# Performance work log

Measured on AMD Instinct MI355X. Metric: run time of the kernel, lower is better.

The kernel has to match this reference:

```python
import jax, jax.numpy as jnp
import numpy as np
from jax import lax

B, N, M = 2, 16384, 4096
C1, C2 = 128, 256
H1, H2 = 256, 128  # mlp = [C1+C2, 256, 128]


def setup_inputs() -> dict:
    key = jax.random.key(0)
    ks = jax.random.split(key, 8)
    return {
        "unknown": jax.random.normal(ks[0], (B, N, 3), jnp.float32),
        "known": jax.random.normal(ks[1], (B, M, 3), jnp.float32),
        "unknow_feats": jax.random.normal(ks[2], (B, C1, N), jnp.float32),
        "known_feats": jax.random.normal(ks[3], (B, C2, M), jnp.float32),
        "W1": jax.random.normal(ks[4], (H1, C1 + C2), jnp.float32) * 0.05,
        "b1": jnp.zeros((H1,), jnp.float32),
        "W2": jax.random.normal(ks[5], (H2, H1), jnp.float32) * 0.05,
        "b2": jnp.zeros((H2,), jnp.float32),
    }


def reference(unknown, known, unknow_feats, known_feats, W1, b1, W2, b2):
    # Pairwise squared distances (B, n, m) via ||a||^2 + ||b||^2 - 2 a.b
    d2 = (
        jnp.sum(unknown * unknown, -1)[:, :, None]
        + jnp.sum(known * known, -1)[:, None, :]
        - 2.0 * jnp.einsum("bnd,bmd->bnm", unknown, known)
    )
    # 3 nearest neighbors
    neg_d2, idx = lax.top_k(-d2, 3)  # (B, n, 3)
    dist = jnp.sqrt(jnp.maximum(-neg_d2, 0.0))  # pointops returns sqrt distances
    dist_recip = 1.0 / (dist + 1e-8)
    weight = dist_recip / jnp.sum(dist_recip, axis=2, keepdims=True)  # (B, n, 3)
    # Gather neighbor features (B, C2, n, 3) and inverse-distance weighted sum
    gathered = jax.vmap(lambda f, i: f[:, i])(known_feats, idx)
    interpolated = jnp.sum(gathered * weight[:, None, :, :], axis=-1)  # (B, C2, n)
    new_features = jnp.concatenate([interpolated, unknow_feats], axis=1)  # (B, C1+C2, n)
    # Shared MLP (1x1 convs, bn=False -> conv bias + ReLU)
    h = jax.nn.relu(jnp.einsum("oc,bcn->bon", W1, new_features) + b1[None, :, None])
    out = jax.nn.relu(jnp.einsum("oc,bcn->bon", W2, h) + b2[None, :, None])
    return out  # (B, mlp[-1], n)
```

## Files before the change

### kernel.cpp

```cpp
#include <hip/hip_runtime.h>
#include <hip/hip_bf16.h>

#define BB 2
#define NN 16384
#define MM 4096
#define C1 128
#define C2 256
#define CIN 384
#define H1 256
#define H2 128
#define XROW 392
#define HROW 264

typedef __attribute__((ext_vector_type(8))) short bf16x8;
typedef __attribute__((ext_vector_type(4))) float f32x4;
typedef __attribute__((ext_vector_type(2))) float f32x2;
typedef __attribute__((ext_vector_type(8))) float f32x8;

__device__ __forceinline__ short f32_to_bf16(float x) {
    unsigned u = __float_as_uint(x);
    u += 0x7fffu + ((u >> 16) & 1u);
    return (short)(u >> 16);
}
__device__ __forceinline__ float bf16_to_f32(unsigned short u) {
    union { unsigned u; float f; } c; c.u = ((unsigned)u) << 16; return c.f;
}
__device__ __forceinline__ unsigned pack_bf16x2(float a, float b) {
    __hip_bfloat162 h = __float22bfloat162_rn(make_float2(a, b));
    union { __hip_bfloat162 h; unsigned u; } cv;
    cv.h = h;
    return cv.u;
}
__device__ __forceinline__ f32x2 score2(f32x2 ax2, f32x2 ay2, f32x2 az2,
                                        f32x2 kx, f32x2 ky, f32x2 kz, f32x2 kn) {
    f32x2 t = ay2 * ky;
    t = __builtin_elementwise_fma(ax2, kx, t);
    t = __builtin_elementwise_fma(az2, kz, t);
    return t + kn;
}

__global__ __launch_bounds__(256) void prep_kernel(
    const float* __restrict__ KF, unsigned short* __restrict__ KT16,
    const float* __restrict__ W1, const float* __restrict__ W2,
    short* __restrict__ W1b, short* __restrict__ W2b,
    const float* __restrict__ known, float* __restrict__ kpk8)
{
    const int bx  = blockIdx.x;
    const int tid = threadIdx.x;
    if (bx < 2048) {
        __shared__ float tl[32][33];
        const int b  = bx >> 10;
        const int c0 = ((bx >> 7) & 7) * 32;
        const int m0 = (bx & 127) * 32;
        const int tx = tid & 31;
        const int ty = tid >> 5;
        #pragma unroll
        for (int r = 0; r < 4; ++r) {
            int c = ty + r * 8;
            tl[c][tx] = KF[((size_t)b * C2 + c0 + c) * MM + m0 + tx];
        }
        __syncthreads();
        #pragma unroll
        for (int r = 0; r < 4; ++r) {
            int m = ty + r * 8;
            KT16[((size_t)b * MM + m0 + m) * C2 + c0 + tx] =
                (unsigned short)f32_to_bf16(tl[tx][m]);
        }
    } else if (bx < 2432) {
        int i = (bx - 2048) * 256 + tid;
        if (i < H1 * CIN) W1b[i] = f32_to_bf16(W1[i]);
        if (i < H2 * H1)  W2b[i] = f32_to_bf16(W2[i]);
    } else {
        int i = (bx - 2432) * 256 + tid;
        if (i < BB * MM) {
            float x = known[3 * i + 0], y = known[3 * i + 1], z = known[3 * i + 2];
            float n = fmaf(x, x, fmaf(y, y, z * z));
            int g = i >> 1, j = i & 1;
            float* base = kpk8 + (size_t)g * 8;
            base[0 + j] = x; base[2 + j] = y; base[4 + j] = z; base[6 + j] = n;
        }
    }
}

__global__ __launch_bounds__(1024, 8) void fused_knn_mlp_kernel(
    const float* __restrict__ unknown,
    const float* __restrict__ kpk8,
    const float* __restrict__ unknow_feats,
    const unsigned short* __restrict__ KT16,
    const short* __restrict__ W1b, const float* __restrict__ b1,
    const short* __restrict__ W2b, const float* __restrict__ b2,
    float* __restrict__ out)
{
    __shared__ float pdv[16][64][3];
    __shared__ float vf[64];
    __shared__ float msc[64][8];
    __shared__ int   mid[64][8];
    __shared__ int   cnt[64];
    __shared__ int   IsL[64 * 3];
    __shared__ float WsL[64 * 3];
    __shared__ short XH[32][XROW];
    __shared__ short Hs[32][HROW];

    const int bx    = blockIdx.x;
    const int tid   = threadIdx.x;
    const int lane  = tid & 63;
    const int w     = __builtin_amdgcn_readfirstlane(tid >> 6);
    const int b     = bx >> 8;
    const int qbase = (bx & 255) * 64;
    const int n     = qbase + lane;

    if (tid < 64) cnt[tid] = 0;

    {
        const float ux = unknown[((size_t)b * NN + n) * 3 + 0];
        const float uy = unknown[((size_t)b * NN + n) * 3 + 1];
        const float uz = unknown[((size_t)b * NN + n) * 3 + 2];
        const f32x2 ax2 = {-2.f * ux, -2.f * ux};
        const f32x2 ay2 = {-2.f * uy, -2.f * uy};
        const f32x2 az2 = {-2.f * uz, -2.f * uz};
        const float un = fmaf(ux, ux, fmaf(uy, uy, uz * uz));

        const int gbase = w * 128;
        const float* __restrict__ kp = kpk8 + ((size_t)b * (MM / 2) + gbase) * 8;

        float va0 = 3e38f, va1 = 3e38f, va2 = 3e38f;
        float vb0 = 3e38f, vb1 = 3e38f, vb2 = 3e38f;
        #pragma unroll 4
        for (int g = 0; g < 128; ++g) {
            const f32x8 G = *(const f32x8*)(kp + (size_t)g * 8);
            const f32x2 kx = __builtin_shufflevector(G, G, 0, 1);
            const f32x2 ky = __builtin_shufflevector(G, G, 2, 3);
            const f32x2 kz = __builtin_shufflevector(G, G, 4, 5);
            const f32x2 kn = __builtin_shufflevector(G, G, 6, 7);
            const f32x2 sc2 = score2(ax2, ay2, az2, kx, ky, kz, kn);
            float sa = sc2.x;
            va2 = __builtin_amdgcn_fmed3f(va1, sa, va2);
            va1 = __builtin_amdgcn_fmed3f(va0, sa, va1);
            va0 = fminf(sa, va0);
            float sb = sc2.y;
            vb2 = __builtin_amdgcn_fmed3f(vb1, sb, vb2);
            vb1 = __builtin_amdgcn_fmed3f(vb0, sb, vb1);
            vb0 = fminf(sb, vb0);
        }
        {
            float bv[3] = {vb0, vb1, vb2};
            #pragma unroll
            for (int k = 0; k < 3; ++k) {
                float d = bv[k];
                va2 = __builtin_amdgcn_fmed3f(va1, d, va2);
                va1 = __builtin_amdgcn_fmed3f(va0, d, va1);
                va0 = fminf(d, va0);
            }
        }
        pdv[w][lane][0] = va0; pdv[w][lane][1] = va1; pdv[w][lane][2] = va2;
        __syncthreads();

        if (tid < 64) {
            float r0 = 3e38f, r1 = 3e38f, r2 = 3e38f;
            #pragma unroll
            for (int ww = 0; ww < 16; ++ww) {
                #pragma unroll
                for (int k = 0; k < 3; ++k) {
                    float d = pdv[ww][tid][k];
                    r2 = __builtin_amdgcn_fmed3f(r1, d, r2);
                    r1 = __builtin_amdgcn_fmed3f(r0, d, r1);
                    r0 = fminf(d, r0);
                }
            }
            vf[tid] = r2;
        }
        __syncthreads();

        const float v2f = vf[lane];
        #pragma unroll 4
        for (int g = 0; g < 128; ++g) {
            const f32x8 G = *(const f32x8*)(kp + (size_t)g * 8);
            const f32x2 kx = __builtin_shufflevector(G, G, 0, 1);
            const f32x2 ky = __builtin_shufflevector(G, G, 2, 3);
            const f32x2 kz = __builtin_shufflevector(G, G, 4, 5);
            const f32x2 kn = __builtin_shufflevector(G, G, 6, 7);
            const f32x2 sc2 = score2(ax2, ay2, az2, kx, ky, kz, kn);
            if (fminf(sc2.x, sc2.y) <= v2f) {
                if (sc2.x <= v2f) {
                    int c = atomicAdd(&cnt[lane], 1);
                    if (c < 8) { msc[lane][c] = sc2.x; mid[lane][c] = (gbase + g) * 2; }
                }
                if (sc2.y <= v2f) {
                    int c = atomicAdd(&cnt[lane], 1);
                    if (c < 8) { msc[lane][c] = sc2.y; mid[lane][c] = (gbase + g) * 2 + 1; }
                }
            }
        }
        __syncthreads();

        if (tid < 64) {
            const int c = cnt[tid] < 8 ? cnt[tid] : 8;
            float r0 = 3e38f, r1 = 3e38f, r2 = 3e38f;
            int   q0 = 0x7FFFFFFF, q1 = 0x7FFFFFFF, q2 = 0x7FFFFFFF;
            #pragma unroll
            for (int k = 0; k < 8; ++k) {
                float d = (k < c) ? msc[tid][k] : 3e38f;
                int   j = (k < c) ? mid[tid][k] : 0x7FFFFFFF;
                const bool lt0 = (d < r0) || (d == r0 && j < q0);
                const bool lt1 = (d < r1) || (d == r1 && j < q1);
                const bool lt2 = (d < r2) || (d == r2 && j < q2);
                float nr2 = lt1 ? r1 : (lt2 ? d : r2);
                int   nq2 = lt1 ? q1 : (lt2 ? j : q2);
                float nr1 = lt0 ? r0 : (lt1 ? d : r1);
                int   nq1 = lt0 ? q0 : (lt1 ? j : q1);
                float nr0 = lt0 ? d : r0;
                int   nq0 = lt0 ? j : q0;
                r0 = nr0; r1 = nr1; r2 = nr2; q0 = nq0; q1 = nq1; q2 = nq2;
            }
            float d0 = sqrtf(fmaxf(r0 + un, 0.f));
            float d1 = sqrtf(fmaxf(r1 + un, 0.f));
            float d2 = sqrtf(fmaxf(r2 + un, 0.f));
            float i0 = 1.f / (d0 + 1e-8f);
            float i1 = 1.f / (d1 + 1e-8f);
            float i2 = 1.f / (d2 + 1e-8f);
            float s  = i0 + i1 + i2;
            IsL[tid * 3 + 0] = q0; IsL[tid * 3 + 1] = q1; IsL[tid * 3 + 2] = q2;
            WsL[tid * 3 + 0] = i0 / s; WsL[tid * 3 + 1] = i1 / s; WsL[tid * 3 + 2] = i2 / s;
        }
    }
    __syncthreads();

    const unsigned short* KTb = KT16 + (size_t)b * MM * C2;
    const int lr = lane & 15;
    const int lq = lane >> 4;
    const int c4 = lane << 2;

    for (int tile = 0; tile < 2; ++tile) {
        const int pbase = tile * 32;

        {
            ushort4 g[2][3];
            #pragma unroll
            for (int j = 0; j < 2; ++j) {
                const int pi = (pbase + 2 * w + j) * 3;
                g[j][0] = *(const ushort4*)(KTb + (size_t)IsL[pi + 0] * C2 + c4);
                g[j][1] = *(const ushort4*)(KTb + (size_t)IsL[pi + 1] * C2 + c4);
                g[j][2] = *(const ushort4*)(KTb + (size_t)IsL[pi + 2] * C2 + c4);
            }
            #pragma unroll
            for (int j = 0; j < 2; ++j) {
                const int pl = 2 * w + j;
                const int pi = (pbase + pl) * 3;
                const float w0 = WsL[pi + 0], w1 = WsL[pi + 1], w2 = WsL[pi + 2];
                float vx = fmaf(w0, bf16_to_f32(g[j][0].x), fmaf(w1, bf16_to_f32(g[j][1].x), w2 * bf16_to_f32(g[j][2].x)));
                float vy = fmaf(w0, bf16_to_f32(g[j][0].y), fmaf(w1, bf16_to_f32(g[j][1].y), w2 * bf16_to_f32(g[j][2].y)));
                float vz = fmaf(w0, bf16_to_f32(g[j][0].z), fmaf(w1, bf16_to_f32(g[j][1].z), w2 * bf16_to_f32(g[j][2].z)));
                float vw = fmaf(w0, bf16_to_f32(g[j][0].w), fmaf(w1, bf16_to_f32(g[j][1].w), w2 * bf16_to_f32(g[j][2].w)));
                uint2 pk;
                pk.x = pack_bf16x2(vx, vy);
                pk.y = pack_bf16x2(vz, vw);
                *(uint2*)&XH[pl][c4] = pk;
            }
            const float* UFb = unknow_feats + (size_t)b * C1 * NN + qbase + pbase;
            const int cc = tid >> 3;
            const int nq = (tid & 7) << 2;
            const float4 f = *(const float4*)(UFb + (size_t)cc * NN + nq);
            XH[nq + 0][C2 + cc] = f32_to_bf16(f.x);
            XH[nq + 1][C2 + cc] = f32_to_bf16(f.y);
            XH[nq + 2][C2 + cc] = f32_to_bf16(f.z);
            XH[nq + 3][C2 + cc] = f32_to_bf16(f.w);
        }
        __syncthreads();

        f32x4 acc1[2];
        acc1[0] = (f32x4){0.f, 0.f, 0.f, 0.f};
        acc1[1] = (f32x4){0.f, 0.f, 0.f, 0.f};
        #pragma unroll 4
        for (int k0 = 0; k0 < CIN; k0 += 32) {
            bf16x8 a  = *(const bf16x8*)(W1b + (size_t)(w * 16 + lr) * CIN + k0 + lq * 8);
            bf16x8 x0 = *(bf16x8*)&XH[lr][k0 + lq * 8];
            bf16x8 x1 = *(bf16x8*)&XH[16 + lr][k0 + lq * 8];
            acc1[0] = __builtin_amdgcn_mfma_f32_16x16x32_bf16(a, x0, acc1[0], 0, 0, 0);
            acc1[1] = __builtin_amdgcn_mfma_f32_16x16x32_bf16(a, x1, acc1[1], 0, 0, 0);
        }
        {
            const int ob = w * 16 + lq * 4;
            float bb0 = b1[ob + 0], bb1 = b1[ob + 1], bb2 = b1[ob + 2], bb3 = b1[ob + 3];
            #pragma unroll
            for (int p = 0; p < 2; ++p) {
                uint2 pk;
                pk.x = pack_bf16x2(fmaxf(acc1[p].x + bb0, 0.f),
                                   fmaxf(acc1[p].y + bb1, 0.f));
                pk.y = pack_bf16x2(fmaxf(acc1[p].z + bb2, 0.f),
                                   fmaxf(acc1[p].w + bb3, 0.f));
                *(uint2*)&Hs[p * 16 + lr][ob] = pk;
            }
        }
        __syncthreads();

        {
            const int r0 = (w & 7) * 16;
            const int pg = (w >> 3) * 16;
            f32x4 acc2 = (f32x4){0.f, 0.f, 0.f, 0.f};
            #pragma unroll 4
            for (int k0 = 0; k0 < H1; k0 += 32) {
                bf16x8 a2 = *(const bf16x8*)(W2b + (size_t)(r0 + lr) * H1 + k0 + lq * 8);
                bf16x8 h  = *(bf16x8*)&Hs[pg + lr][k0 + lq * 8];
                acc2 = __builtin_amdgcn_mfma_f32_16x16x32_bf16(a2, h, acc2, 0, 0, 0);
            }
            const int nn = qbase + pbase + pg + lr;
            #pragma unroll
            for (int r = 0; r < 4; ++r) {
                const int o = r0 + lq * 4 + r;
                out[((size_t)b * H2 + o) * NN + nn] =
                    fmaxf(((const float*)&acc2)[r] + b2[o], 0.f);
            }
        }
        __syncthreads();
    }
}

extern "C" void kernel_launch(void* const* d_in, const int* in_sizes, int n_in,
                              void* d_out, int out_size, void* d_ws, size_t ws_size,
                              hipStream_t stream) {
    const float* unknown      = (const float*)d_in[0];
    const float* known        = (const float*)d_in[1];
    const float* unknow_feats = (const float*)d_in[2];
    const float* known_feats  = (const float*)d_in[3];
    const float* W1           = (const float*)d_in[4];
    const float* b1           = (const float*)d_in[5];
    const float* W2           = (const float*)d_in[6];
    const float* b2           = (const float*)d_in[7];
    float* out = (float*)d_out;

    char* ws = (char*)d_ws;
    short*          W1b  = (short*)(ws);
    short*          W2b  = (short*)(ws + 196608);
    float*          kpk8 = (float*)(ws + 262144);
    unsigned short* KT16 = (unsigned short*)(ws + 393216);

    prep_kernel<<<2464, 256, 0, stream>>>(
        known_feats, KT16, W1, W2, W1b, W2b, known, kpk8);

    fused_knn_mlp_kernel<<<512, 1024, 0, stream>>>(
        unknown, kpk8, unknow_feats, KT16, W1b, b1, W2b, b2, out);
}
```

Before: 162.5 us.

## Halve block to 512 threads, alias LDS buffers, prefetch unknown features early

The fused kNN+MLP kernel moves from 1024 to 512 threads per block. Each wave now scans 256 known-point pairs instead of 128, gathers 4 points instead of 2, and computes 32 output rows per MFMA tile in the first layer. The kNN scratch, the XH input tile and the hidden activations now share one LDS union, and Hs is dropped by writing H into XH after an extra barrier. Unknown features for both tiles are prefetched into registers at kernel start so their load latency overlaps the kNN search. This lowers LDS footprint and may allow more blocks per CU, at the cost of more registers per thread and longer serial work per wave.

After: 176.7 us. 8.7% more time.

```diff
diff --git a/kernel.cpp b/kernel.cpp
--- a/kernel.cpp
+++ b/kernel.cpp
@@ -10,7 +10,6 @@
 #define H1 256
 #define H2 128
 #define XROW 392
-#define HROW 264
 
 typedef __attribute__((ext_vector_type(8))) short bf16x8;
 typedef __attribute__((ext_vector_type(4))) float f32x4;
@@ -82,7 +81,7 @@
     }
 }
 
-__global__ __launch_bounds__(1024, 8) void fused_knn_mlp_kernel(
+__global__ __launch_bounds__(512, 8) void fused_knn_mlp_kernel(
     const float* __restrict__ unknown,
     const float* __restrict__ kpk8,
     const float* __restrict__ unknow_feats,
@@ -91,15 +90,19 @@
     const short* __restrict__ W2b, const float* __restrict__ b2,
     float* __restrict__ out)
 {
-    __shared__ float pdv[16][64][3];
-    __shared__ float vf[64];
-    __shared__ float msc[64][8];
-    __shared__ int   mid[64][8];
-    __shared__ int   cnt[64];
+    union SharedU {
+        struct {
+            float pdv[8][64][3];
+            float vf[64];
+            float msc[64][8];
+            int   mid[64][8];
+            int   cnt[64];
+        } p1;
+        short XH[32][XROW];
+    };
+    __shared__ SharedU S;
     __shared__ int   IsL[64 * 3];
     __shared__ float WsL[64 * 3];
-    __shared__ short XH[32][XROW];
-    __shared__ short Hs[32][HROW];
 
     const int bx    = blockIdx.x;
     const int tid   = threadIdx.x;
@@ -109,7 +112,19 @@
     const int qbase = (bx & 255) * 64;
     const int n     = qbase + lane;
 
-    if (tid < 64) cnt[tid] = 0;
+    float4 uf[4];
+    {
+        const float* UFb = unknow_feats + (size_t)b * C1 * NN + qbase;
+        #pragma unroll
+        for (int i = 0; i < 4; ++i) {
+            int e  = (i & 1) * 512 + tid;
+            int cc = e >> 3;
+            int nq = ((e & 7) << 2) + (i >> 1) * 32;
+            uf[i] = *(const float4*)(UFb + (size_t)cc * NN + nq);
+        }
+    }
+
+    if (tid < 64) S.p1.cnt[tid] = 0;
 
     {
         const float ux = unknown[((size_t)b * NN + n) * 3 + 0];
@@ -120,13 +135,13 @@
         const f32x2 az2 = {-2.f * uz, -2.f * uz};
         const float un = fmaf(ux, ux, fmaf(uy, uy, uz * uz));
 
-        const int gbase = w * 128;
+        const int gbase = w * 256;
         const float* __restrict__ kp = kpk8 + ((size_t)b * (MM / 2) + gbase) * 8;
 
         float va0 = 3e38f, va1 = 3e38f, va2 = 3e38f;
         float vb0 = 3e38f, vb1 = 3e38f, vb2 = 3e38f;
         #pragma unroll 4
-        for (int g = 0; g < 128; ++g) {
+        for (int g = 0; g < 256; ++g) {
             const f32x8 G = *(const f32x8*)(kp + (size_t)g * 8);
             const f32x2 kx = __builtin_shufflevector(G, G, 0, 1);
             const f32x2 ky = __builtin_shufflevector(G, G, 2, 3);
@@ -152,28 +167,28 @@
                 va0 = fminf(d, va0);
             }
         }
-        pdv[w][lane][0] = va0; pdv[w][lane][1] = va1; pdv[w][lane][2] = va2;
+        S.p1.pdv[w][lane][0] = va0; S.p1.pdv[w][lane][1] = va1; S.p1.pdv[w][lane][2] = va2;
         __syncthreads();
 
         if (tid < 64) {
             float r0 = 3e38f, r1 = 3e38f, r2 = 3e38f;
             #pragma unroll
-            for (int ww = 0; ww < 16; ++ww) {
+            for (int ww = 0; ww < 8; ++ww) {
                 #pragma unroll
                 for (int k = 0; k < 3; ++k) {
-                    float d = pdv[ww][tid][k];
+                    float d = S.p1.pdv[ww][tid][k];
                     r2 = __builtin_amdgcn_fmed3f(r1, d, r2);
                     r1 = __builtin_amdgcn_fmed3f(r0, d, r1);
                     r0 = fminf(d, r0);
                 }
             }
-            vf[tid] = r2;
-        }
-        __syncthreads();
-
-        const float v2f = vf[lane];
+            S.p1.vf[tid] = r2;
+        }
+        __syncthreads();
+
+        const float v2f = S.p1.vf[lane];
         #pragma unroll 4
-        for (int g = 0; g < 128; ++g) {
+        for (int g = 0; g < 256; ++g) {
             const f32x8 G = *(const f32x8*)(kp + (size_t)g * 8);
             const f32x2 kx = __builtin_shufflevector(G, G, 0, 1);
             const f32x2 ky = __builtin_shufflevector(G, G, 2, 3);
@@ -182,25 +197,25 @@
             const f32x2 sc2 = score2(ax2, ay2, az2, kx, ky, kz, kn);
             if (fminf(sc2.x, sc2.y) <= v2f) {
                 if (sc2.x <= v2f) {
-                    int c = atomicAdd(&cnt[lane], 1);
-                    if (c < 8) { msc[lane][c] = sc2.x; mid[lane][c] = (gbase + g) * 2; }
+                    int c = atomicAdd(&S.p1.cnt[lane], 1);
+                    if (c < 8) { S.p1.msc[lane][c] = sc2.x; S.p1.mid[lane][c] = (gbase + g) * 2; }
                 }
                 if (sc2.y <= v2f) {
-                    int c = atomicAdd(&cnt[lane], 1);
-                    if (c < 8) { msc[lane][c] = sc2.y; mid[lane][c] = (gbase + g) * 2 + 1; }
+                    int c = atomicAdd(&S.p1.cnt[lane], 1);
+                    if (c < 8) { S.p1.msc[lane][c] = sc2.y; S.p1.mid[lane][c] = (gbase + g) * 2 + 1; }
                 }
             }
         }
         __syncthreads();
 
         if (tid < 64) {
-            const int c = cnt[tid] < 8 ? cnt[tid] : 8;
+            const int c = S.p1.cnt[tid] < 8 ? S.p1.cnt[tid] : 8;
             float r0 = 3e38f, r1 = 3e38f, r2 = 3e38f;
             int   q0 = 0x7FFFFFFF, q1 = 0x7FFFFFFF, q2 = 0x7FFFFFFF;
             #pragma unroll
             for (int k = 0; k < 8; ++k) {
-                float d = (k < c) ? msc[tid][k] : 3e38f;
-                int   j = (k < c) ? mid[tid][k] : 0x7FFFFFFF;
+                float d = (k < c) ? S.p1.msc[tid][k] : 3e38f;
+                int   j = (k < c) ? S.p1.mid[tid][k] : 0x7FFFFFFF;
                 const bool lt0 = (d < r0) || (d == r0 && j < q0);
                 const bool lt1 = (d < r1) || (d == r1 && j < q1);
                 const bool lt2 = (d < r2) || (d == r2 && j < q2);
@@ -234,17 +249,28 @@
         const int pbase = tile * 32;
 
         {
-            ushort4 g[2][3];
-            #pragma unroll
-            for (int j = 0; j < 2; ++j) {
-                const int pi = (pbase + 2 * w + j) * 3;
+            ushort4 g[4][3];
+            #pragma unroll
+            for (int j = 0; j < 4; ++j) {
+                const int pi = (pbase + 4 * w + j) * 3;
                 g[j][0] = *(const ushort4*)(KTb + (size_t)IsL[pi + 0] * C2 + c4);
                 g[j][1] = *(const ushort4*)(KTb + (size_t)IsL[pi + 1] * C2 + c4);
                 g[j][2] = *(const ushort4*)(KTb + (size_t)IsL[pi + 2] * C2 + c4);
             }
             #pragma unroll
-            for (int j = 0; j < 2; ++j) {
-                const int pl = 2 * w + j;
+            for (int i = 0; i < 2; ++i) {
+                const float4 f = uf[tile * 2 + i];
+                int e  = i * 512 + tid;
+                int cc = e >> 3;
+                int nq = (e & 7) << 2;
+                S.XH[nq + 0][C2 + cc] = f32_to_bf16(f.x);
+                S.XH[nq + 1][C2 + cc] = f32_to_bf16(f.y);
+                S.XH[nq + 2][C2 + cc] = f32_to_bf16(f.z);
+                S.XH[nq + 3][C2 + cc] = f32_to_bf16(f.w);
+            }
+            #pragma unroll
+            for (int j = 0; j < 4; ++j) {
+                const int pl = 4 * w + j;
                 const int pi = (pbase + pl) * 3;
                 const float w0 = WsL[pi + 0], w1 = WsL[pi + 1], w2 = WsL[pi + 2];
                 float vx = fmaf(w0, bf16_to_f32(g[j][0].x), fmaf(w1, bf16_to_f32(g[j][1].x), w2 * bf16_to_f32(g[j][2].x)));
@@ -254,61 +280,70 @@
                 uint2 pk;
                 pk.x = pack_bf16x2(vx, vy);
                 pk.y = pack_bf16x2(vz, vw);
-                *(uint2*)&XH[pl][c4] = pk;
-            }
-            const float* UFb = unknow_feats + (size_t)b * C1 * NN + qbase + pbase;
-            const int cc = tid >> 3;
-            const int nq = (tid & 7) << 2;
-            const float4 f = *(const float4*)(UFb + (size_t)cc * NN + nq);
-            XH[nq + 0][C2 + cc] = f32_to_bf16(f.x);
-            XH[nq + 1][C2 + cc] = f32_to_bf16(f.y);
-            XH[nq + 2][C2 + cc] = f32_to_bf16(f.z);
-            XH[nq + 3][C2 + cc] = f32_to_bf16(f.w);
-        }
-        __syncthreads();
-
-        f32x4 acc1[2];
-        acc1[0] = (f32x4){0.f, 0.f, 0.f, 0.f};
-        acc1[1] = (f32x4){0.f, 0.f, 0.f, 0.f};
+                *(uint2*)&S.XH[pl][c4] = pk;
+            }
+        }
+        __syncthreads();
+
+        f32x4 acc1[2][2];
+        #pragma unroll
+        for (int t = 0; t < 2; ++t)
+            #pragma unroll
+            for (int p = 0; p < 2; ++p) acc1[t][p] = (f32x4){0.f, 0.f, 0.f, 0.f};
         #pragma unroll 4
         for (int k0 = 0; k0 < CIN; k0 += 32) {
-            bf16x8 a  = *(const bf16x8*)(W1b + (size_t)(w * 16 + lr) * CIN + k0 + lq * 8);
-            bf16x8 x0 = *(bf16x8*)&XH[lr][k0 + lq * 8];
-            bf16x8 x1 = *(bf16x8*)&XH[16 + lr][k0 + lq * 8];
-            acc1[0] = __builtin_amdgcn_mfma_f32_16x16x32_bf16(a, x0, acc1[0], 0, 0, 0);
-            acc1[1] = __builtin_amdgcn_mfma_f32_16x16x32_bf16(a, x1, acc1[1], 0, 0, 0);
-        }
-        {
-            const int ob = w * 16 + lq * 4;
+            bf16x8 a[2], x[2];
+            #pragma unroll
+            for (int t = 0; t < 2; ++t)
+                a[t] = *(const bf16x8*)(W1b + (size_t)(w * 32 + t * 16 + lr) * CIN + k0 + lq * 8);
+            #pragma unroll
+            for (int p = 0; p < 2; ++p)
+                x[p] = *(bf16x8*)&S.XH[p * 16 + lr][k0 + lq * 8];
+            #pragma unroll
+            for (int t = 0; t < 2; ++t)
+                #pragma unroll
+                for (int p = 0; p < 2; ++p)
+                    acc1[t][p] = __builtin_amdgcn_mfma_f32_16x16x32_bf16(a[t], x[p], acc1[t][p], 0, 0, 0);
+        }
+        __syncthreads();
+
+        #pragma unroll
+        for (int t = 0; t < 2; ++t) {
+            const int ob = w * 32 + t * 16 + lq * 4;
             float bb0 = b1[ob + 0], bb1 = b1[ob + 1], bb2 = b1[ob + 2], bb3 = b1[ob + 3];
             #pragma unroll
             for (int p = 0; p < 2; ++p) {
                 uint2 pk;
-                pk.x = pack_bf16x2(fmaxf(acc1[p].x + bb0, 0.f),
-                                   fmaxf(acc1[p].y + bb1, 0.f));
-                pk.y = pack_bf16x2(fmaxf(acc1[p].z + bb2, 0.f),
-                                   fmaxf(acc1[p].w + bb3, 0.f));
-                *(uint2*)&Hs[p * 16 + lr][ob] = pk;
+                pk.x = pack_bf16x2(fmaxf(acc1[t][p].x + bb0, 0.f),
+                                   fmaxf(acc1[t][p].y + bb1, 0.f));
+                pk.y = pack_bf16x2(fmaxf(acc1[t][p].z + bb2, 0.f),
+                                   fmaxf(acc1[t][p].w + bb3, 0.f));
+                *(uint2*)&S.XH[p * 16 + lr][ob] = pk;
             }
         }
         __syncthreads();
 
         {
-            const int r0 = (w & 7) * 16;
-            const int pg = (w >> 3) * 16;
-            f32x4 acc2 = (f32x4){0.f, 0.f, 0.f, 0.f};
+            f32x4 acc2[2];
+            acc2[0] = (f32x4){0.f, 0.f, 0.f, 0.f};
+            acc2[1] = (f32x4){0.f, 0.f, 0.f, 0.f};
             #pragma unroll 4
             for (int k0 = 0; k0 < H1; k0 += 32) {
-                bf16x8 a2 = *(const bf16x8*)(W2b + (size_t)(r0 + lr) * H1 + k0 + lq * 8);
-                bf16x8 h  = *(bf16x8*)&Hs[pg + lr][k0 + lq * 8];
-                acc2 = __builtin_amdgcn_mfma_f32_16x16x32_bf16(a2, h, acc2, 0, 0, 0);
-            }
-            const int nn = qbase + pbase + pg + lr;
-            #pragma unroll
-            for (int r = 0; r < 4; ++r) {
-                const int o = r0 + lq * 4 + r;
-                out[((size_t)b * H2 + o) * NN + nn] =
-                    fmaxf(((const float*)&acc2)[r] + b2[o], 0.f);
+                bf16x8 a2 = *(const bf16x8*)(W2b + (size_t)(w * 16 + lr) * H1 + k0 + lq * 8);
+                bf16x8 h0 = *(bf16x8*)&S.XH[lr][k0 + lq * 8];
+                bf16x8 h1 = *(bf16x8*)&S.XH[16 + lr][k0 + lq * 8];
+                acc2[0] = __builtin_amdgcn_mfma_f32_16x16x32_bf16(a2, h0, acc2[0], 0, 0, 0);
+                acc2[1] = __builtin_amdgcn_mfma_f32_16x16x32_bf16(a2, h1, acc2[1], 0, 0, 0);
+            }
+            #pragma unroll
+            for (int p = 0; p < 2; ++p) {
+                const int nn = qbase + pbase + p * 16 + lr;
+                #pragma unroll
+                for (int r = 0; r < 4; ++r) {
+                    const int o = w * 16 + lq * 4 + r;
+                    out[((size_t)b * H2 + o) * NN + nn] =
+                        fmaxf(((const float*)&acc2[p])[r] + b2[o], 0.f);
+                }
             }
         }
         __syncthreads();
@@ -337,6 +372,6 @@
     prep_kernel<<<2464, 256, 0, stream>>>(
         known_feats, KT16, W1, W2, W1b, W2b, known, kpk8);
 
-    fused_knn_mlp_kernel<<<512, 1024, 0, stream>>>(
+    fused_knn_mlp_kernel<<<512, 512, 0, stream>>>(
         unknown, kpk8, unknow_feats, KT16, W1b, b1, W2b, b2, out);
 }
```

## Prefetch unknown features and next-tile neighbor gathers to overlap with MFMA

Applied to the files above, without the earlier changes.

The unknow_feats loads for both tiles now happen at kernel start, so their latency overlaps the kNN search. The neighbor-feature gathers for the second tile are issued right after the first tile's barrier and hide behind the first tile's MLP MFMAs. This removes exposed global-memory latency from the per-tile critical path. In exchange it keeps more values live in registers, which may raise VGPR pressure and reduce occupancy.

After: 163.9 us. Within noise of the previous version (+0.9%).

```diff
diff --git a/kernel.cpp b/kernel.cpp
--- a/kernel.cpp
+++ b/kernel.cpp
@@ -109,6 +109,16 @@
     const int qbase = (bx & 255) * 64;
     const int n     = qbase + lane;
 
+    float4 uf[2];
+    {
+        const float* UFb = unknow_feats + (size_t)b * C1 * NN + qbase;
+        const int cc = tid >> 3;
+        const int nq = (tid & 7) << 2;
+        #pragma unroll
+        for (int t = 0; t < 2; ++t)
+            uf[t] = *(const float4*)(UFb + (size_t)cc * NN + t * 32 + nq);
+    }
+
     if (tid < 64) cnt[tid] = 0;
 
     {
@@ -230,42 +240,52 @@
     const int lq = lane >> 4;
     const int c4 = lane << 2;
 
+    ushort4 gcur[2][3], gnext[2][3];
+    #pragma unroll
+    for (int j = 0; j < 2; ++j) {
+        const int pi = (2 * w + j) * 3;
+        gcur[j][0] = *(const ushort4*)(KTb + (size_t)IsL[pi + 0] * C2 + c4);
+        gcur[j][1] = *(const ushort4*)(KTb + (size_t)IsL[pi + 1] * C2 + c4);
+        gcur[j][2] = *(const ushort4*)(KTb + (size_t)IsL[pi + 2] * C2 + c4);
+    }
+
     for (int tile = 0; tile < 2; ++tile) {
         const int pbase = tile * 32;
 
         {
-            ushort4 g[2][3];
-            #pragma unroll
-            for (int j = 0; j < 2; ++j) {
-                const int pi = (pbase + 2 * w + j) * 3;
-                g[j][0] = *(const ushort4*)(KTb + (size_t)IsL[pi + 0] * C2 + c4);
-                g[j][1] = *(const ushort4*)(KTb + (size_t)IsL[pi + 1] * C2 + c4);
-                g[j][2] = *(const ushort4*)(KTb + (size_t)IsL[pi + 2] * C2 + c4);
-            }
             #pragma unroll
             for (int j = 0; j < 2; ++j) {
                 const int pl = 2 * w + j;
                 const int pi = (pbase + pl) * 3;
                 const float w0 = WsL[pi + 0], w1 = WsL[pi + 1], w2 = WsL[pi + 2];
-                float vx = fmaf(w0, bf16_to_f32(g[j][0].x), fmaf(w1, bf16_to_f32(g[j][1].x), w2 * bf16_to_f32(g[j][2].x)));
-                float vy = fmaf(w0, bf16_to_f32(g[j][0].y), fmaf(w1, bf16_to_f32(g[j][1].y), w2 * bf16_to_f32(g[j][2].y)));
-                float vz = fmaf(w0, bf16_to_f32(g[j][0].z), fmaf(w1, bf16_to_f32(g[j][1].z), w2 * bf16_to_f32(g[j][2].z)));
-                float vw = fmaf(w0, bf16_to_f32(g[j][0].w), fmaf(w1, bf16_to_f32(g[j][1].w), w2 * bf16_to_f32(g[j][2].w)));
+                float vx = fmaf(w0, bf16_to_f32(gcur[j][0].x), fmaf(w1, bf16_to_f32(gcur[j][1].x), w2 * bf16_to_f32(gcur[j][2].x)));
+                float vy = fmaf(w0, bf16_to_f32(gcur[j][0].y), fmaf(w1, bf16_to_f32(gcur[j][1].y), w2 * bf16_to_f32(gcur[j][2].y)));
+                float vz = fmaf(w0, bf16_to_f32(gcur[j][0].z), fmaf(w1, bf16_to_f32(gcur[j][1].z), w2 * bf16_to_f32(gcur[j][2].z)));
+                float vw = fmaf(w0, bf16_to_f32(gcur[j][0].w), fmaf(w1, bf16_to_f32(gcur[j][1].w), w2 * bf16_to_f32(gcur[j][2].w)));
                 uint2 pk;
                 pk.x = pack_bf16x2(vx, vy);
                 pk.y = pack_bf16x2(vz, vw);
                 *(uint2*)&XH[pl][c4] = pk;
             }
-            const float* UFb = unknow_feats + (size_t)b * C1 * NN + qbase + pbase;
+            const float4 f = uf[tile];
             const int cc = tid >> 3;
             const int nq = (tid & 7) << 2;
-            const float4 f = *(const float4*)(UFb + (size_t)cc * NN + nq);
             XH[nq + 0][C2 + cc] = f32_to_bf16(f.x);
             XH[nq + 1][C2 + cc] = f32_to_bf16(f.y);
             XH[nq + 2][C2 + cc] = f32_to_bf16(f.z);
             XH[nq + 3][C2 + cc] = f32_to_bf16(f.w);
         }
         __syncthreads();
+
+        if (tile == 0) {
+            #pragma unroll
+            for (int j = 0; j < 2; ++j) {
+                const int pi = (32 + 2 * w + j) * 3;
+                gnext[j][0] = *(const ushort4*)(KTb + (size_t)IsL[pi + 0] * C2 + c4);
+                gnext[j][1] = *(const ushort4*)(KTb + (size_t)IsL[pi + 1] * C2 + c4);
+                gnext[j][2] = *(const ushort4*)(KTb + (size_t)IsL[pi + 2] * C2 + c4);
+            }
+        }
 
         f32x4 acc1[2];
         acc1[0] = (f32x4){0.f, 0.f, 0.f, 0.f};
@@ -312,6 +332,11 @@
             }
         }
         __syncthreads();
+
+        #pragma unroll
+        for (int j = 0; j < 2; ++j)
+            #pragma unroll
+            for (int k = 0; k < 3; ++k) gcur[j][k] = gnext[j][k];
     }
 }
 
```
